# Optimization experiments

Hardware: AMD Instinct MI355X
Metric: run time of the kernel (lower is better)

The kernel has to match this reference:

```python
import jax, jax.numpy as jnp
import numpy as np
import math

# Static config (matches init_kwargs): C4 rotation group, 14x14 grid
B = 2
CIN = 96
MID = 96
HEADS = 8
COUT = 96
G = 4            # group elements (0/90/180/270 deg rotations)
S = 14           # spatial size == max_pos_embedding
HID = 16         # hidden width of the row/col embedding MLP (Conv2d 1->16)
DPOS = MID // 3                  # 32: row / col embedding dims
DG = MID - 2 * DPOS              # 32: group embedding dim


def setup_inputs() -> dict:
    key = jax.random.key(0)
    ks = jax.random.split(key, 12)

    def lin(k, shape, scale):
        return jax.random.normal(k, shape, jnp.float32) * scale

    x = jax.random.normal(ks[0], (B, CIN, G, S, S), jnp.float32)
    # 1x1x1 Conv3d weights == per-position linear layers [out, in]
    Wq = lin(ks[1], (MID * HEADS, CIN), 1.0 / np.sqrt(CIN)); bq = jnp.zeros((MID * HEADS,), jnp.float32)
    Wk = lin(ks[2], (MID * HEADS, CIN), 1.0 / np.sqrt(CIN)); bk = jnp.zeros((MID * HEADS,), jnp.float32)
    Wv = lin(ks[3], (MID * HEADS, CIN), 1.0 / np.sqrt(CIN)); bv = jnp.zeros((MID * HEADS,), jnp.float32)
    Wo = lin(ks[4], (COUT, MID * HEADS), 1.0 / np.sqrt(MID * HEADS)); bo = jnp.zeros((COUT,), jnp.float32)
    # row embedding MLP: scalar -> 16 -> LayerNorm -> Swish -> DPOS
    rw1 = lin(ks[5], (HID,), 1.0); rb1 = jnp.zeros((HID,), jnp.float32)
    rgam = jnp.ones((HID,), jnp.float32); rbet = jnp.zeros((HID,), jnp.float32)
    rw2 = lin(ks[6], (HID, DPOS), 1.0 / np.sqrt(HID)); rb2 = jnp.zeros((DPOS,), jnp.float32)
    # col embedding MLP
    cw1 = lin(ks[7], (HID,), 1.0); cb1 = jnp.zeros((HID,), jnp.float32)
    cgam = jnp.ones((HID,), jnp.float32); cbet = jnp.zeros((HID,), jnp.float32)
    cw2 = lin(ks[8], (HID, DPOS), 1.0 / np.sqrt(HID)); cb2 = jnp.zeros((DPOS,), jnp.float32)
    # group element embedding table
    gemb = lin(ks[9], (G, DG), 0.02)

    # Relative-position buffers: rel coordinate (k-i)/(S-1) in [-1,1], rotated by
    # each group element (left action of the rotation on R^2).  [G, S, S, S, S]
    d = (jnp.arange(S)[None, :] - jnp.arange(S)[:, None]).astype(jnp.float32) / (S - 1)
    dr = jnp.broadcast_to(d[:, None, :, None], (S, S, S, S))   # row offset (k-i)
    dc = jnp.broadcast_to(d[None, :, None, :], (S, S, S, S))   # col offset (l-j)
    ang = jnp.arange(G, dtype=jnp.float32) * (np.pi / 2.0)
    cs = jnp.cos(ang)[:, None, None, None, None]
    sn = jnp.sin(ang)[:, None, None, None, None]
    row_rel = cs * dr - sn * dc
    col_rel = sn * dr + cs * dc
    # relative group-element indices acted on by each group element v: [G, G, G]
    gi = jnp.arange(G)
    g_idx = (gi[None, None, :] - gi[None, :, None] + gi[:, None, None]) % G

    return {"x": x, "Wq": Wq, "bq": bq, "Wk": Wk, "bk": bk, "Wv": Wv, "bv": bv,
            "Wo": Wo, "bo": bo,
            "rw1": rw1, "rb1": rb1, "rgam": rgam, "rbet": rbet, "rw2": rw2, "rb2": rb2,
            "cw1": cw1, "cb1": cb1, "cgam": cgam, "cbet": cbet, "cw2": cw2, "cb2": cb2,
            "gemb": gemb, "row_rel": row_rel, "col_rel": col_rel, "g_idx": g_idx}


def _embed(rel, w1, b1, gam, bet, w2, b2):
    # Conv2d(1->16, k=1) + channel LayerNorm + Swish + Conv2d(16->DPOS, k=1)
    h = rel[..., None] * w1 + b1                                   # [..., 16]
    mu = jnp.mean(h, axis=-1, keepdims=True)
    var = jnp.var(h, axis=-1, keepdims=True)
    h = (h - mu) / jnp.sqrt(var + 1e-5) * gam + bet
    h = h * jax.nn.sigmoid(h)                                      # Swish
    return h @ w2 + b2                                             # [..., DPOS]


def reference(x, Wq, bq, Wk, bk, Wv, bv, Wo, bo,
              rw1, rb1, rgam, rbet, rw2, rb2,
              cw1, cb1, cgam, cbet, cw2, cb2,
              gemb, row_rel, col_rel, g_idx):
    b = x.shape[0]

    def proj(W, bias):
        y = jnp.einsum('bcgij,dc->bdgij', x, W) + bias[None, :, None, None, None]
        return y.reshape(b, MID, HEADS, G, S, S)   # split channels as (mid, heads)

    q = proj(Wq, bq)
    k = proj(Wk, bk)
    v = proj(Wv, bv)

    q_row = q[:, :DPOS]
    q_col = q[:, DPOS:2 * DPOS]
    q_grp = q[:, 2 * DPOS:]

    row_e = _embed(row_rel, rw1, rb1, rgam, rbet, rw2, rb2)        # [G,S,S,S,S,DPOS]
    col_e = _embed(col_rel, cw1, cb1, cgam, cbet, cw2, cb2)

    row_s = jnp.einsum('bchgij,vijklc->bhvgijkl', q_row, row_e)
    col_s = jnp.einsum('bchgij,vijklc->bhvgijkl', q_col, col_e)
    g_s = jnp.einsum('bchgij,vgmc->bhvgijm', q_grp, gemb[g_idx])
    content = jnp.einsum('bchgij,bchmkl->bhgijmkl', q, k)

    # broadcast add into [b, h, v, g, i, j, m, k, l]
    scores = (jnp.expand_dims(row_s + col_s, -3)
              + g_s[..., None, None]
              + content[:, :, None]) / math.sqrt(CIN)

    sh = scores.shape
    probs = jax.nn.softmax(scores.reshape(sh[:-3] + (-1,)), axis=-1).reshape(sh)

    vo = jnp.einsum('bhvgijmkl,bchmkl->bchvij', probs, v)
    vo = vo.reshape(b, MID * HEADS, G, S, S)
    return jnp.einsum('bcgij,dc->bdgij', vo, Wo) + bo[None, :, None, None, None]
```

## Files before the change

kernel.cpp:

```cpp
#include <hip/hip_runtime.h>
#include <hip/hip_bf16.h>

constexpr int kB   = 2;
constexpr int kH   = 8;
constexpr int kG   = 4;
constexpr int kS   = 14;
constexpr int kSS  = 196;
constexpr int kKey = 784;
constexpr int kKeyP = 800;
constexpr int kMid = 96;
constexpr int kQR  = 28;
constexpr int kCL  = 788;
constexpr int kTS  = 36;
constexpr float kScl = 0.10206207261596577f;
constexpr float kK2  = 0.14724663682f;
constexpr float kCc  = 11.5415603272f;

typedef __attribute__((ext_vector_type(8))) short bf16x8;
typedef __attribute__((ext_vector_type(4))) float f32x4;

constexpr size_t SZ_QKb = (size_t)kB*kH*kG*kSS*kMid/2;
constexpr size_t OFF_Qb = 0;
constexpr size_t OFF_Kb = OFF_Qb + SZ_QKb;
constexpr size_t OFF_V  = OFF_Kb + SZ_QKb;
constexpr size_t SZ_V   = (size_t)kB*kH*kMid*kKeyP/2;
constexpr size_t OFF_FR = OFF_V + SZ_V;
constexpr size_t OFF_FC = OFF_FR + 27*32;
constexpr size_t OFF_PS = OFF_FC + 27*32;
constexpr size_t SZ_PS  = (size_t)kB*kH*kG*kSS*kKeyP/2;
constexpr size_t OFF_WOH = OFF_PS + SZ_PS;

__global__ __launch_bounds__(256)
void k_qkv(const float* __restrict__ x,
           const float* __restrict__ Wq, const float* __restrict__ bq,
           const float* __restrict__ Wk, const float* __restrict__ bk,
           const float* __restrict__ Wv, const float* __restrict__ bv,
           __hip_bfloat16* __restrict__ Qb, __hip_bfloat16* __restrict__ Kb,
           __hip_bfloat16* __restrict__ Vb,
           const float* __restrict__ rw1, const float* __restrict__ rb1,
           const float* __restrict__ rgam, const float* __restrict__ rbet,
           const float* __restrict__ rw2, const float* __restrict__ rb2,
           const float* __restrict__ cw1, const float* __restrict__ cb1,
           const float* __restrict__ cgam, const float* __restrict__ cbet,
           const float* __restrict__ cw2, const float* __restrict__ cb2,
           float* __restrict__ frow, float* __restrict__ fcol,
           const float* __restrict__ Wo, __hip_bfloat16* __restrict__ Woh,
           float* __restrict__ out0) {
  const int bid = blockIdx.x;
  const int ten = blockIdx.y;
  const int i = bid % 14;
  const int g = (bid / 14) % 4;
  const int b = bid / 56;
  const float* W    = (ten == 0) ? Wq : (ten == 1) ? Wk : Wv;
  const float* bias = (ten == 0) ? bq : (ten == 1) ? bk : bv;

  {
    int zidx = (ten*112 + bid)*256 + threadIdx.x;
    if (zidx < 37632) ((float4*)out0)[zidx] = make_float4(0.f, 0.f, 0.f, 0.f);
  }

  __shared__ alignas(16) float xs[14][100];
  for (int idx = threadIdx.x; idx < 96*14; idx += 256) {
    int cin = idx / 14, j = idx % 14;
    xs[j][cin] = x[((size_t)(b*96 + cin)*4 + g)*196 + i*14 + j];
  }
  __syncthreads();

  for (int d = threadIdx.x; d < 768; d += 256) {
    int c = d >> 3, h = d & 7;
    float bvv = bias[d];
    float acc[14];
#pragma unroll
    for (int j = 0; j < 14; ++j) acc[j] = bvv;
    const float* wrow = W + (size_t)d * 96;
    for (int cc = 0; cc < 96; cc += 4) {
      float4 w = *(const float4*)(wrow + cc);
#pragma unroll
      for (int j = 0; j < 14; ++j) {
        float4 xv = *(const float4*)(&xs[j][cc]);
        acc[j] += w.x*xv.x + w.y*xv.y + w.z*xv.z + w.w*xv.w;
      }
    }
    if (ten == 2) {
      __hip_bfloat16* op = Vb + ((size_t)((b*8 + h)*96 + c))*kKeyP + g*196 + i*14;
#pragma unroll
      for (int j = 0; j < 14; ++j) op[j] = __float2bfloat16(acc[j]);
    } else {
      __hip_bfloat16* dst = (ten == 0) ? Qb : Kb;
      __hip_bfloat16* op = dst + ((size_t)((b*8 + h)*4 + g)*196 + i*14)*96 + c;
#pragma unroll
      for (int j = 0; j < 14; ++j) op[(size_t)j*96] = __float2bfloat16(acc[j]);
    }
  }

  if (ten == 1) {
    for (int idx = bid*256 + threadIdx.x; idx < 73728; idx += 112*256) {
      int h = idx / 9216, rem = idx - h*9216;
      int d = rem / 96, c = rem - d*96;
      Woh[idx] = __float2bfloat16(Wo[(size_t)d*768 + c*8 + h]);
    }
  }
  if (ten == 2 && bid < 16) {
    for (int idx = threadIdx.x; idx < 96*16; idx += 256) {
      int c = idx >> 4, kp = idx & 15;
      Vb[((size_t)(bid*96 + c))*kKeyP + kKey + kp] = __float2bfloat16(0.f);
    }
  }
  if (ten == 0 && bid == 0 && threadIdx.x < 54) {
    int t = threadIdx.x;
    int which = t / 27;
    int n = t % 27;
    float tv = (float)(n - 13) / 13.0f;
    const float* w1  = which ? cw1  : rw1;
    const float* b1  = which ? cb1  : rb1;
    const float* gam = which ? cgam : rgam;
    const float* bet = which ? cbet : rbet;
    const float* w2  = which ? cw2  : rw2;
    const float* b2  = which ? cb2  : rb2;
    float h[16];
    float mu = 0.f;
#pragma unroll
    for (int d = 0; d < 16; ++d) { h[d] = tv * w1[d] + b1[d]; mu += h[d]; }
    mu *= (1.0f/16.0f);
    float var = 0.f;
#pragma unroll
    for (int d = 0; d < 16; ++d) { float z = h[d] - mu; var += z*z; }
    var *= (1.0f/16.0f);
    float rstd = rsqrtf(var + 1e-5f);
#pragma unroll
    for (int d = 0; d < 16; ++d) {
      float z = (h[d] - mu) * rstd * gam[d] + bet[d];
      h[d] = z / (1.0f + expf(-z));
    }
    float* outp = (which ? fcol : frow) + n*32;
    for (int c = 0; c < 32; ++c) {
      float o = b2[c];
#pragma unroll
      for (int d = 0; d < 16; ++d) o += h[d] * w2[d*32 + c];
      outp[c] = o;
    }
  }
}

__global__ __launch_bounds__(512, 4)
void k_attn(const __hip_bfloat16* __restrict__ Qb, const __hip_bfloat16* __restrict__ Kb,
            const float* __restrict__ frow_g, const float* __restrict__ fcol_g,
            const float* __restrict__ gemb_g, __hip_bfloat16* __restrict__ Pb) {
  const int tid = threadIdx.x;
  const int bid = blockIdx.x;
  const int jhalf = bid & 1;
  const int t2 = bid >> 1;
  const int qi = t2 % 14;
  const int hh = (t2 / 14) % 8;
  const int bb = t2 / 112;
  const int bh = bb*8 + hh;

  __shared__ alignas(16) float qs[kQR][96];
  __shared__ alignas(16) float frowS[27*kTS];
  __shared__ alignas(16) float fcolS[27*kTS];
  __shared__ alignas(16) float gembS[4*kTS];
  __shared__ alignas(16) float ArrE[kQR][28];
  __shared__ alignas(16) float AclE[kQR][28];
  __shared__ alignas(16) float AgEall[4][kQR][4];
  __shared__ float T[kQR][14];
  __shared__ float DinvS[kQR];
  __shared__ alignas(16) __hip_bfloat16 contl[kQR][kCL];

  const short* Qs = (const short*)Qb;
  const short* Ks = (const short*)Kb;

  for (int idx = tid; idx < kQR*96; idx += 512) {
    int q = idx / 96, c = idx - q*96;
    int g = q / 7, jq = q - g*7;
    qs[q][c] = __bfloat162float(
        Qb[((size_t)((bh*4 + g)*kSS + qi*14 + jhalf*7 + jq))*96 + c]);
  }
  for (int idx = tid; idx < 864; idx += 512) {
    int s = idx >> 5, c = idx & 31;
    frowS[s*kTS + c] = frow_g[idx] * kK2;
    fcolS[s*kTS + c] = fcol_g[idx] * kK2;
  }
  if (tid < 128) gembS[(tid >> 5)*kTS + (tid & 31)] = gemb_g[tid] * kK2;
  __syncthreads();

  {
    const int lane = tid & 63;
    const int wave = tid >> 6;
    const int col  = lane & 15;
    const int quad = lane >> 4;

    bf16x8 afrag[2][3];
#pragma unroll
    for (int mt = 0; mt < 2; ++mt) {
      int m = mt*16 + col;
      int q = (m < kQR) ? m : 0;
      const short* qrow = Qs +
          ((size_t)((bh*4 + q/7)*kSS + qi*14 + jhalf*7 + q%7))*96;
#pragma unroll
      for (int ks = 0; ks < 3; ++ks)
        afrag[mt][ks] = *(const bf16x8*)(qrow + ks*32 + quad*8);
    }

    for (int nt = wave; nt < 49; nt += 8) {
      int kl = nt*16 + col;
      const short* krow = Ks + ((size_t)(bh*kKey + kl))*96;
      bf16x8 b0 = *(const bf16x8*)(krow + 0*32 + quad*8);
      bf16x8 b1 = *(const bf16x8*)(krow + 1*32 + quad*8);
      bf16x8 b2 = *(const bf16x8*)(krow + 2*32 + quad*8);
      f32x4 c0 = {0.f,0.f,0.f,0.f};
      f32x4 c1 = {0.f,0.f,0.f,0.f};
      c0 = __builtin_amdgcn_mfma_f32_16x16x32_bf16(afrag[0][0], b0, c0, 0, 0, 0);
      c0 = __builtin_amdgcn_mfma_f32_16x16x32_bf16(afrag[0][1], b1, c0, 0, 0, 0);
      c0 = __builtin_amdgcn_mfma_f32_16x16x32_bf16(afrag[0][2], b2, c0, 0, 0, 0);
      c1 = __builtin_amdgcn_mfma_f32_16x16x32_bf16(afrag[1][0], b0, c1, 0, 0, 0);
      c1 = __builtin_amdgcn_mfma_f32_16x16x32_bf16(afrag[1][1], b1, c1, 0, 0, 0);
      c1 = __builtin_amdgcn_mfma_f32_16x16x32_bf16(afrag[1][2], b2, c1, 0, 0, 0);
      int ijn = kl % 196, mk = kl / 196;
#pragma unroll
      for (int r = 0; r < 4; ++r) {
        int q0 = quad*4 + r;
        contl[q0][ijn*4 + mk] = __float2bfloat16(exp2f(c0[r]*kK2 - kCc));
        int q1 = 16 + quad*4 + r;
        if (q1 < kQR)
          contl[q1][ijn*4 + mk] = __float2bfloat16(exp2f(c1[r]*kK2 - kCc));
      }
    }
  }

  for (int t = tid; t < kQR*58; t += 512) {
    int q = t / 58, s = t - q*58;
    float acc = 0.f;
    if (s < 27) {
#pragma unroll
      for (int c = 0; c < 32; ++c) acc += qs[q][c] * frowS[s*kTS + c];
      ArrE[q][s] = exp2f(acc);
    } else if (s < 54) {
      int n = s - 27;
#pragma unroll
      for (int c = 0; c < 32; ++c) acc += qs[q][32+c] * fcolS[n*kTS + c];
      AclE[q][n] = exp2f(acc);
    } else {
      int p = s - 54;
#pragma unroll
      for (int c = 0; c < 32; ++c) acc += qs[q][64+c] * gembS[p*kTS + c];
      float e = exp2f(acc);
      int gq = q / 7;
#pragma unroll
      for (int vv = 0; vv < 4; ++vv)
        AgEall[vv][q][(p + gq - vv + 8) & 3] = e;
    }
  }
  __syncthreads();

  const int actv = (tid < 392);
  const int qB  = actv ? (tid / 14) : 0;
  const int kkB = actv ? (tid % 14) : 0;
  const int jlB = jhalf*7 + (qB % 7);
  const int daB = kkB - qi;
  const int half = actv ? (tid / 196) : 0;
  const int ijC  = actv ? (tid % 196) : 0;
  const int kkC = ijC / 14;
  const int llC = ijC % 14;
  const int daC = kkC - qi;

#pragma unroll
  for (int v = 0; v < 4; ++v) {
    const int s1a = (v==0) ? 1 : (v==2) ? -1 : 0;
    const int s1b = (v==1) ? -1 : (v==3) ? 1 : 0;
    const int s2a = (v==1) ? 1 : (v==3) ? -1 : 0;
    const int s2b = (v==0) ? 1 : (v==2) ? -1 : 0;

    if (actv) {
      f32x4 ag = *(const f32x4*)(&AgEall[v][qB][0]);
      float Rk = s1a ? ArrE[qB][13 + s1a*daB] : AclE[qB][13 + s2a*daB];
      float acc = 0.f;
#pragma unroll
      for (int ll = 0; ll < 14; ++ll) {
        const int db = ll - jlB;
        float Cl = s1a ? AclE[qB][13 + s2b*db] : ArrE[qB][13 + s1b*db];
        ushort4 u = *(const ushort4*)(&contl[qB][(kkB*14 + ll)*4]);
        float e0 = __uint_as_float((unsigned)u.x << 16);
        float e1 = __uint_as_float((unsigned)u.y << 16);
        float e2 = __uint_as_float((unsigned)u.z << 16);
        float e3 = __uint_as_float((unsigned)u.w << 16);
        acc += Cl * (e0*ag.x + e1*ag.y + e2*ag.z + e3*ag.w);
      }
      T[qB][kkB] = Rk * acc;
    }
    __syncthreads();
    if (tid < kQR) {
      float dsum = 0.f;
#pragma unroll
      for (int kk = 0; kk < 14; ++kk) dsum += T[tid][kk];
      DinvS[tid] = 1.0f / dsum;
    }
    __syncthreads();

    if (actv) {
      __hip_bfloat16* pbase =
          Pb + ((size_t)((bh*4 + v)*kSS + qi*14 + jhalf*7))*kKeyP + half*392 + ijC;
#pragma unroll
      for (int jq = 0; jq < 7; ++jq) {
        const int db = llC - (jhalf*7 + jq);
        const int ai = s1a*daC + s1b*db, ci = s2a*daC + s2b*db;
        float am0 = 0.f, am1 = 0.f;
#pragma unroll
        for (int gq = 0; gq < 4; ++gq) {
          const int q = gq*7 + jq;
          const float fq = ArrE[q][13 + ai] * AclE[q][13 + ci] * DinvS[q];
          ushort2 u = *(const ushort2*)(&contl[q][ijC*4 + half*2]);
          float e0 = __uint_as_float((unsigned)u.x << 16);
          float e1 = __uint_as_float((unsigned)u.y << 16);
          am0 += e0 * (AgEall[v][q][half*2]     * fq);
          am1 += e1 * (AgEall[v][q][half*2 + 1] * fq);
        }
        __hip_bfloat16* pp = pbase + (size_t)jq*kKeyP;
        pp[0]   = __float2bfloat16(am0);
        pp[196] = __float2bfloat16(am1);
      }
    }
    if (tid < 112) {
      int jq = tid >> 4, kp = tid & 15;
      Pb[((size_t)((bh*4 + v)*kSS + qi*14 + jhalf*7 + jq))*kKeyP + kKey + kp] =
          __float2bfloat16(0.f);
    }
  }
}

__global__ __launch_bounds__(128)
void k_pv(const __hip_bfloat16* __restrict__ Pb,
          const __hip_bfloat16* __restrict__ Vb,
          const __hip_bfloat16* __restrict__ Woh,
          const float* __restrict__ bo, float* __restrict__ out) {
  const int tid  = threadIdx.x;
  const int lane = tid & 63;
  const int wave = tid >> 6;
  const int bh = blockIdx.x / 49;
  const int mt = blockIdx.x % 49;
  const int mrow = lane & 15;
  const int quad = lane >> 4;
  const int b_ = bh >> 3, h_ = bh & 7;

  __shared__ alignas(16) __hip_bfloat16 vos[16][104];

  {
    const short* Ap = (const short*)Pb +
        ((size_t)(bh*kKey + mt*16 + mrow))*kKeyP + quad*8;
    const short* Bp = (const short*)Vb + ((size_t)bh*96)*kKeyP + quad*8;

    f32x4 acc0 = {0.f,0.f,0.f,0.f};
    f32x4 acc1 = {0.f,0.f,0.f,0.f};
    f32x4 acc2 = {0.f,0.f,0.f,0.f};
    const int n0 = (wave*3 + 0)*16 + mrow;
    const int n1 = (wave*3 + 1)*16 + mrow;
    const int n2 = (wave*3 + 2)*16 + mrow;

    for (int ks = 0; ks < kKeyP/32; ++ks) {
      bf16x8 a  = *(const bf16x8*)(Ap + ks*32);
      bf16x8 b0 = *(const bf16x8*)(Bp + (size_t)n0*kKeyP + ks*32);
      bf16x8 b1 = *(const bf16x8*)(Bp + (size_t)n1*kKeyP + ks*32);
      bf16x8 b2 = *(const bf16x8*)(Bp + (size_t)n2*kKeyP + ks*32);
      acc0 = __builtin_amdgcn_mfma_f32_16x16x32_bf16(a, b0, acc0, 0, 0, 0);
      acc1 = __builtin_amdgcn_mfma_f32_16x16x32_bf16(a, b1, acc1, 0, 0, 0);
      acc2 = __builtin_amdgcn_mfma_f32_16x16x32_bf16(a, b2, acc2, 0, 0, 0);
    }
#pragma unroll
    for (int r = 0; r < 4; ++r) {
      vos[quad*4 + r][n0] = __float2bfloat16(acc0[r]);
      vos[quad*4 + r][n1] = __float2bfloat16(acc1[r]);
      vos[quad*4 + r][n2] = __float2bfloat16(acc2[r]);
    }
  }
  __syncthreads();

  const short* wb = (const short*)Woh + (size_t)h_*9216;
#pragma unroll
  for (int w = 0; w < 3; ++w) {
    const int dt = wave*3 + w;
    f32x4 acc = {0.f,0.f,0.f,0.f};
#pragma unroll
    for (int ks = 0; ks < 3; ++ks) {
      bf16x8 a  = *(const bf16x8*)(&vos[mrow][ks*32 + quad*8]);
      bf16x8 bf = *(const bf16x8*)(wb + (size_t)(dt*16 + mrow)*96 + ks*32 + quad*8);
      acc = __builtin_amdgcn_mfma_f32_16x16x32_bf16(a, bf, acc, 0, 0, 0);
    }
    const int d = dt*16 + mrow;
    const float bias = (h_ == 0) ? bo[d] : 0.f;
#pragma unroll
    for (int r = 0; r < 4; ++r) {
      int m = mt*16 + quad*4 + r;
      int v = m / kSS, ij = m - v*kSS;
      atomicAdd(&out[((size_t)(b_*96 + d)*4 + v)*kSS + ij], acc[r] + bias);
    }
  }
}

extern "C" void kernel_launch(void* const* d_in, const int* in_sizes, int n_in,
                              void* d_out, int out_size, void* d_ws, size_t ws_size,
                              hipStream_t stream) {
  const float* x    = (const float*)d_in[0];
  const float* Wq   = (const float*)d_in[1];
  const float* bq   = (const float*)d_in[2];
  const float* Wk   = (const float*)d_in[3];
  const float* bk   = (const float*)d_in[4];
  const float* Wv   = (const float*)d_in[5];
  const float* bv   = (const float*)d_in[6];
  const float* Wo   = (const float*)d_in[7];
  const float* bo   = (const float*)d_in[8];
  const float* rw1  = (const float*)d_in[9];
  const float* rb1  = (const float*)d_in[10];
  const float* rgam = (const float*)d_in[11];
  const float* rbet = (const float*)d_in[12];
  const float* rw2  = (const float*)d_in[13];
  const float* rb2  = (const float*)d_in[14];
  const float* cw1  = (const float*)d_in[15];
  const float* cb1  = (const float*)d_in[16];
  const float* cgam = (const float*)d_in[17];
  const float* cbet = (const float*)d_in[18];
  const float* cw2  = (const float*)d_in[19];
  const float* cb2  = (const float*)d_in[20];
  const float* gemb = (const float*)d_in[21];

  float* ws = (float*)d_ws;
  __hip_bfloat16* Qb = (__hip_bfloat16*)(ws + OFF_Qb);
  __hip_bfloat16* Kb = (__hip_bfloat16*)(ws + OFF_Kb);
  __hip_bfloat16* Vb = (__hip_bfloat16*)(ws + OFF_V);
  float* Frow = ws + OFF_FR;
  float* Fcol = ws + OFF_FC;
  __hip_bfloat16* Pb = (__hip_bfloat16*)(ws + OFF_PS);
  __hip_bfloat16* Woh = (__hip_bfloat16*)(ws + OFF_WOH);
  float* out  = (float*)d_out;

  k_qkv<<<dim3(112, 3), 256, 0, stream>>>(x, Wq, bq, Wk, bk, Wv, bv, Qb, Kb, Vb,
                                          rw1, rb1, rgam, rbet, rw2, rb2,
                                          cw1, cb1, cgam, cbet, cw2, cb2,
                                          Frow, Fcol, Wo, Woh, out);
  k_attn<<<448, 512, 0, stream>>>(Qb, Kb, Frow, Fcol, gemb, Pb);
  k_pv<<<784, 128, 0, stream>>>(Pb, Vb, Woh, bo, out);
}
```

Before: 202.3 us.

## Fuse PV and output projection into attention kernel, keep probabilities in LDS

The attention kernel now keeps its bf16 probability tile in shared memory and immediately multiplies it by V and then by the output projection with MFMA, atomically accumulating into the output. This removes the separate k_pv launch and the write and re-read of the large probability buffer in global memory. In exchange, each block streams the whole V slice for its head from global/L2 (re-read by 14*2 blocks per head), uses more LDS via pooled buffers, and lowers the occupancy hint to 2 blocks per CU.

```diff
diff --git a/kernel.cpp b/kernel.cpp
--- a/kernel.cpp
+++ b/kernel.cpp
@@ -12,6 +12,7 @@
 constexpr int kQR  = 28;
 constexpr int kCL  = 788;
 constexpr int kTS  = 36;
+constexpr int kPAS = 808;
 constexpr float kScl = 0.10206207261596577f;
 constexpr float kK2  = 0.14724663682f;
 constexpr float kCc  = 11.5415603272f;
@@ -26,9 +27,7 @@
 constexpr size_t SZ_V   = (size_t)kB*kH*kMid*kKeyP/2;
 constexpr size_t OFF_FR = OFF_V + SZ_V;
 constexpr size_t OFF_FC = OFF_FR + 27*32;
-constexpr size_t OFF_PS = OFF_FC + 27*32;
-constexpr size_t SZ_PS  = (size_t)kB*kH*kG*kSS*kKeyP/2;
-constexpr size_t OFF_WOH = OFF_PS + SZ_PS;
+constexpr size_t OFF_WOH = OFF_FC + 27*32;
 
 __global__ __launch_bounds__(256)
 void k_qkv(const float* __restrict__ x,
@@ -142,10 +141,13 @@
   }
 }
 
-__global__ __launch_bounds__(512, 4)
+__global__ __launch_bounds__(512, 2)
 void k_attn(const __hip_bfloat16* __restrict__ Qb, const __hip_bfloat16* __restrict__ Kb,
             const float* __restrict__ frow_g, const float* __restrict__ fcol_g,
-            const float* __restrict__ gemb_g, __hip_bfloat16* __restrict__ Pb) {
+            const float* __restrict__ gemb_g,
+            const __hip_bfloat16* __restrict__ Vb,
+            const __hip_bfloat16* __restrict__ Woh,
+            const float* __restrict__ bo, float* __restrict__ out) {
   const int tid = threadIdx.x;
   const int bid = blockIdx.x;
   const int jhalf = bid & 1;
@@ -155,16 +157,21 @@
   const int bb = t2 / 112;
   const int bh = bb*8 + hh;
 
-  __shared__ alignas(16) float qs[kQR][96];
-  __shared__ alignas(16) float frowS[27*kTS];
-  __shared__ alignas(16) float fcolS[27*kTS];
-  __shared__ alignas(16) float gembS[4*kTS];
+  __shared__ alignas(16) char poolA[32*kPAS*2];
+  __shared__ alignas(16) char poolB[kQR*kCL*2];
   __shared__ alignas(16) float ArrE[kQR][28];
   __shared__ alignas(16) float AclE[kQR][28];
   __shared__ alignas(16) float AgEall[4][kQR][4];
   __shared__ float T[kQR][14];
   __shared__ float DinvS[kQR];
-  __shared__ alignas(16) __hip_bfloat16 contl[kQR][kCL];
+
+  float (*qs)[96] = (float(*)[96])poolA;
+  float* frowS = (float*)(poolA + 10752);
+  float* fcolS = (float*)(poolA + 10752 + 3888);
+  float* gembS = (float*)(poolA + 10752 + 2*3888);
+  __hip_bfloat16 (*pA)[kPAS] = (__hip_bfloat16(*)[kPAS])poolA;
+  __hip_bfloat16 (*contl)[kCL] = (__hip_bfloat16(*)[kCL])poolB;
+  __hip_bfloat16 (*vos)[104]   = (__hip_bfloat16(*)[104])poolB;
 
   const short* Qs = (const short*)Qb;
   const short* Ks = (const short*)Kb;
@@ -251,6 +258,7 @@
     }
   }
   __syncthreads();
+  { int r = tid >> 4, kp = tid & 15; pA[r][784 + kp] = __float2bfloat16(0.f); }
 
   const int actv = (tid < 392);
   const int qB  = actv ? (tid / 14) : 0;
@@ -297,8 +305,6 @@
     __syncthreads();
 
     if (actv) {
-      __hip_bfloat16* pbase =
-          Pb + ((size_t)((bh*4 + v)*kSS + qi*14 + jhalf*7))*kKeyP + half*392 + ijC;
 #pragma unroll
       for (int jq = 0; jq < 7; ++jq) {
         const int db = llC - (jhalf*7 + jq);
@@ -314,83 +320,69 @@
           am0 += e0 * (AgEall[v][q][half*2]     * fq);
           am1 += e1 * (AgEall[v][q][half*2 + 1] * fq);
         }
-        __hip_bfloat16* pp = pbase + (size_t)jq*kKeyP;
-        pp[0]   = __float2bfloat16(am0);
-        pp[196] = __float2bfloat16(am1);
-      }
-    }
-    if (tid < 112) {
-      int jq = tid >> 4, kp = tid & 15;
-      Pb[((size_t)((bh*4 + v)*kSS + qi*14 + jhalf*7 + jq))*kKeyP + kKey + kp] =
-          __float2bfloat16(0.f);
-    }
-  }
-}
-
-__global__ __launch_bounds__(128)
-void k_pv(const __hip_bfloat16* __restrict__ Pb,
-          const __hip_bfloat16* __restrict__ Vb,
-          const __hip_bfloat16* __restrict__ Woh,
-          const float* __restrict__ bo, float* __restrict__ out) {
-  const int tid  = threadIdx.x;
+        pA[jq*4 + v][half*392 + ijC]       = __float2bfloat16(am0);
+        pA[jq*4 + v][half*392 + 196 + ijC] = __float2bfloat16(am1);
+      }
+    }
+  }
+  __syncthreads();
+
   const int lane = tid & 63;
   const int wave = tid >> 6;
-  const int bh = blockIdx.x / 49;
-  const int mt = blockIdx.x % 49;
-  const int mrow = lane & 15;
+  const int col  = lane & 15;
   const int quad = lane >> 4;
   const int b_ = bh >> 3, h_ = bh & 7;
 
-  __shared__ alignas(16) __hip_bfloat16 vos[16][104];
-
   {
-    const short* Ap = (const short*)Pb +
-        ((size_t)(bh*kKey + mt*16 + mrow))*kKeyP + quad*8;
     const short* Bp = (const short*)Vb + ((size_t)bh*96)*kKeyP + quad*8;
-
-    f32x4 acc0 = {0.f,0.f,0.f,0.f};
-    f32x4 acc1 = {0.f,0.f,0.f,0.f};
-    f32x4 acc2 = {0.f,0.f,0.f,0.f};
-    const int n0 = (wave*3 + 0)*16 + mrow;
-    const int n1 = (wave*3 + 1)*16 + mrow;
-    const int n2 = (wave*3 + 2)*16 + mrow;
-
-    for (int ks = 0; ks < kKeyP/32; ++ks) {
-      bf16x8 a  = *(const bf16x8*)(Ap + ks*32);
-      bf16x8 b0 = *(const bf16x8*)(Bp + (size_t)n0*kKeyP + ks*32);
-      bf16x8 b1 = *(const bf16x8*)(Bp + (size_t)n1*kKeyP + ks*32);
-      bf16x8 b2 = *(const bf16x8*)(Bp + (size_t)n2*kKeyP + ks*32);
-      acc0 = __builtin_amdgcn_mfma_f32_16x16x32_bf16(a, b0, acc0, 0, 0, 0);
-      acc1 = __builtin_amdgcn_mfma_f32_16x16x32_bf16(a, b1, acc1, 0, 0, 0);
-      acc2 = __builtin_amdgcn_mfma_f32_16x16x32_bf16(a, b2, acc2, 0, 0, 0);
-    }
-#pragma unroll
-    for (int r = 0; r < 4; ++r) {
-      vos[quad*4 + r][n0] = __float2bfloat16(acc0[r]);
-      vos[quad*4 + r][n1] = __float2bfloat16(acc1[r]);
-      vos[quad*4 + r][n2] = __float2bfloat16(acc2[r]);
+#pragma unroll
+    for (int tk = 0; tk < 2; ++tk) {
+      int t = wave + tk*8;
+      if (t < 12) {
+        int mt = t / 6, nt = t - mt*6;
+        int crow = nt*16 + col;
+        const short* ap = (const short*)(&pA[mt*16 + col][0]) + quad*8;
+        const short* bp = Bp + (size_t)crow*kKeyP;
+        f32x4 acc = {0.f,0.f,0.f,0.f};
+        for (int ks = 0; ks < 25; ++ks) {
+          bf16x8 a = *(const bf16x8*)(ap + ks*32);
+          bf16x8 b = *(const bf16x8*)(bp + ks*32);
+          acc = __builtin_amdgcn_mfma_f32_16x16x32_bf16(a, b, acc, 0, 0, 0);
+        }
+#pragma unroll
+        for (int r = 0; r < 4; ++r)
+          vos[mt*16 + quad*4 + r][crow] = __float2bfloat16(acc[r]);
+      }
     }
   }
   __syncthreads();
 
-  const short* wb = (const short*)Woh + (size_t)h_*9216;
-#pragma unroll
-  for (int w = 0; w < 3; ++w) {
-    const int dt = wave*3 + w;
-    f32x4 acc = {0.f,0.f,0.f,0.f};
-#pragma unroll
-    for (int ks = 0; ks < 3; ++ks) {
-      bf16x8 a  = *(const bf16x8*)(&vos[mrow][ks*32 + quad*8]);
-      bf16x8 bf = *(const bf16x8*)(wb + (size_t)(dt*16 + mrow)*96 + ks*32 + quad*8);
-      acc = __builtin_amdgcn_mfma_f32_16x16x32_bf16(a, bf, acc, 0, 0, 0);
-    }
-    const int d = dt*16 + mrow;
-    const float bias = (h_ == 0) ? bo[d] : 0.f;
-#pragma unroll
-    for (int r = 0; r < 4; ++r) {
-      int m = mt*16 + quad*4 + r;
-      int v = m / kSS, ij = m - v*kSS;
-      atomicAdd(&out[((size_t)(b_*96 + d)*4 + v)*kSS + ij], acc[r] + bias);
+  {
+    const short* wb = (const short*)Woh + (size_t)h_*9216;
+#pragma unroll
+    for (int tk = 0; tk < 2; ++tk) {
+      int t = wave + tk*8;
+      if (t < 12) {
+        int mt = t / 6, dt = t - mt*6;
+        f32x4 acc = {0.f,0.f,0.f,0.f};
+#pragma unroll
+        for (int ks = 0; ks < 3; ++ks) {
+          bf16x8 a = *(const bf16x8*)(&vos[mt*16 + col][ks*32 + quad*8]);
+          bf16x8 b = *(const bf16x8*)(wb + (size_t)(dt*16 + col)*96 + ks*32 + quad*8);
+          acc = __builtin_amdgcn_mfma_f32_16x16x32_bf16(a, b, acc, 0, 0, 0);
+        }
+        const int d = dt*16 + col;
+        const float bias = (h_ == 0) ? bo[d] : 0.f;
+#pragma unroll
+        for (int r = 0; r < 4; ++r) {
+          int rr = mt*16 + quad*4 + r;
+          if (rr < kQR) {
+            int jq = rr >> 2, vv = rr & 3;
+            int ijq = qi*14 + jhalf*7 + jq;
+            atomicAdd(&out[((size_t)(b_*96 + d)*4 + vv)*kSS + ijq], acc[r] + bias);
+          }
+        }
+      }
     }
   }
 }
@@ -427,7 +419,6 @@
   __hip_bfloat16* Vb = (__hip_bfloat16*)(ws + OFF_V);
   float* Frow = ws + OFF_FR;
   float* Fcol = ws + OFF_FC;
-  __hip_bfloat16* Pb = (__hip_bfloat16*)(ws + OFF_PS);
   __hip_bfloat16* Woh = (__hip_bfloat16*)(ws + OFF_WOH);
   float* out  = (float*)d_out;
 
@@ -435,6 +426,5 @@
                                           rw1, rb1, rgam, rbet, rw2, rb2,
                                           cw1, cb1, cgam, cbet, cw2, cb2,
                                           Frow, Fcol, Wo, Woh, out);
-  k_attn<<<448, 512, 0, stream>>>(Qb, Kb, Frow, Fcol, gemb, Pb);
-  k_pv<<<784, 128, 0, stream>>>(Pb, Vb, Woh, bo, out);
+  k_attn<<<448, 512, 0, stream>>>(Qb, Kb, Frow, Fcol, gemb, Vb, Woh, bo, out);
 }
```

Result: no change. 205.6 us (+1.7%).
